# Performance work log

Hardware: AMD Instinct MI355X
Metric: run time of the kernel (lower is better)

## Reference

```python
import jax, jax.numpy as jnp
import numpy as np

N, F_IN, H, C, E, K = 100000, 128, 512, 16, 3200000, 3
EPS = 1e-5


def setup_inputs() -> dict:
    key = jax.random.key(0)
    ks = jax.random.split(key, 12)
    x = jax.random.normal(ks[0], (N, F_IN), jnp.float32)
    edge_index = jax.random.randint(ks[1], (2, E), 0, N, jnp.int64)
    # TAGConv has K+1 hop linears (bias folded into one vector, like PyG)
    W1 = jax.random.normal(ks[2], (K + 1, F_IN, H), jnp.float32) * 0.02
    b1 = jnp.zeros((H,), jnp.float32)
    W2 = jax.random.normal(ks[3], (K + 1, H, H), jnp.float32) * 0.02
    b2 = jnp.zeros((H,), jnp.float32)
    W3 = jax.random.normal(ks[4], (K + 1, H, C), jnp.float32) * 0.02
    b3 = jnp.zeros((C,), jnp.float32)
    gn1_w = jnp.ones((H,), jnp.float32)
    gn1_b = jnp.zeros((H,), jnp.float32)
    gn1_a = jnp.ones((H,), jnp.float32)  # mean_scale alpha
    gn2_w = jnp.ones((H,), jnp.float32)
    gn2_b = jnp.zeros((H,), jnp.float32)
    gn2_a = jnp.ones((H,), jnp.float32)
    return {"x": x, "edge_index": edge_index,
            "W1": W1, "b1": b1, "W2": W2, "b2": b2, "W3": W3, "b3": b3,
            "gn1_w": gn1_w, "gn1_b": gn1_b, "gn1_a": gn1_a,
            "gn2_w": gn2_w, "gn2_b": gn2_b, "gn2_a": gn2_a}


def _gcn_norm(edge_index, n):
    # PyG TAGConv: gcn_norm with add_self_loops=False, all-ones edge weights
    row, col = edge_index[0], edge_index[1]  # source j, target i
    deg = jax.ops.segment_sum(jnp.ones((edge_index.shape[1],), jnp.float32), col,
                              num_segments=n)
    dinv = jnp.where(deg > 0, jax.lax.rsqrt(jnp.maximum(deg, 1.0)), 0.0)
    return row, col, dinv[row] * dinv[col]


def _prop(h, row, col, norm, n):
    # out[i] = sum_{(j->i)} norm_e * h[j]
    return jax.ops.segment_sum(norm[:, None] * h[row], col, num_segments=n)


def _tagconv(x, row, col, norm, W, b):
    n = x.shape[0]
    out = x @ W[0]
    h = x
    for k in range(1, W.shape[0]):
        h = _prop(h, row, col, norm, n)
        out = out + h @ W[k]
    return out + b


def _graphnorm(x, w, b, a):
    # single graph: per-graph mean/var over all nodes
    mean = jnp.mean(x, axis=0)
    sub = x - a * mean
    var = jnp.mean(sub * sub, axis=0)
    return sub * jax.lax.rsqrt(var + EPS) * w + b


def reference(x, edge_index, W1, b1, W2, b2, W3, b3,
              gn1_w, gn1_b, gn1_a, gn2_w, gn2_b, gn2_a):
    n = x.shape[0]
    row, col, norm = _gcn_norm(edge_index, n)
    h = jax.nn.relu(_tagconv(x, row, col, norm, W1, b1))
    h = _graphnorm(h, gn1_w, gn1_b, gn1_a)
    h = jax.nn.relu(_tagconv(h, row, col, norm, W2, b2))
    h = _graphnorm(h, gn2_w, gn2_b, gn2_a)
    return _tagconv(h, row, col, norm, W3, b3)
```

## Files before the change

kernel.cpp:

```cpp
#include <hip/hip_runtime.h>

#define NN 100000
#define EE 3200000
#define EPSF 1e-5f

typedef unsigned short u16;
typedef short bf16x8 __attribute__((ext_vector_type(8)));
typedef float f32x4 __attribute__((ext_vector_type(4)));

static inline int cdiv(int a, int b) { return (a + b - 1) / b; }

__device__ __forceinline__ float b2f(u16 u) {
    return __uint_as_float((unsigned int)u << 16);
}
__device__ __forceinline__ u16 f2b(float f) {
    unsigned int i = __float_as_uint(f);
    return (u16)((i + 0x7FFFu + ((i >> 16) & 1u)) >> 16);
}
__device__ __forceinline__ int ep_src(unsigned int p) { return (int)(p & 0x1FFFFu); }
__device__ __forceinline__ float ep_w(unsigned int p) {
    return __uint_as_float(p & 0xFFFE0000u);
}
__device__ __forceinline__ unsigned pkhi(float f0, float f1) {
    return __builtin_amdgcn_perm(__float_as_uint(f1), __float_as_uint(f0), 0x07060302u);
}

__global__ void k_init(int* __restrict__ deg, int* __restrict__ cursor,
                       float* __restrict__ stats) {
    int i = blockIdx.x * 256 + threadIdx.x;
    if (i < NN) {
        deg[i] = 0;
        cursor[i] = 0;
    }
    if (i < 2048) stats[i] = 0.f;
}

__global__ void k_deg(const int* __restrict__ col, int* __restrict__ deg) {
    int i = blockIdx.x * 256 + threadIdx.x;
    if (i < EE) atomicAdd(&deg[col[i]], 1);
}

__global__ void k_dinv(const int* __restrict__ deg, float* __restrict__ dinv) {
    int i = blockIdx.x * 256 + threadIdx.x;
    if (i < NN) {
        int d = deg[i];
        dinv[i] = d > 0 ? rsqrtf((float)d) : 0.f;
    }
}

__global__ void k_scan(const int* __restrict__ deg, int* __restrict__ offs) {
    __shared__ int sh[1024];
    int tid = threadIdx.x;
    int start = tid * 98;
    int end = min(start + 98, NN);
    int sum = 0;
    for (int i = start; i < end; ++i) sum += deg[i];
    sh[tid] = sum;
    __syncthreads();
    for (int off = 1; off < 1024; off <<= 1) {
        int t = (tid >= off) ? sh[tid - off] : 0;
        __syncthreads();
        sh[tid] += t;
        __syncthreads();
    }
    int base = tid ? sh[tid - 1] : 0;
    for (int i = start; i < end; ++i) {
        offs[i] = base;
        base += deg[i];
    }
    if (tid == 1023) offs[NN] = sh[1023];
}

__global__ void k_scatter(const int* __restrict__ row, const int* __restrict__ col,
                          const float* __restrict__ dinv, const int* __restrict__ offs,
                          int* __restrict__ cursor, unsigned int* __restrict__ ep) {
    int i = blockIdx.x * 256 + threadIdx.x;
    if (i < EE) {
        int c = col[i], r = row[i];
        int pos = offs[c] + atomicAdd(&cursor[c], 1);
        float w = dinv[r] * dinv[c];
        unsigned int u = __float_as_uint(w);
        unsigned int rb = (u + 0xFFFFu + ((u >> 17) & 1u)) & 0xFFFE0000u;
        ep[pos] = rb | (unsigned int)r;
    }
}

__global__ void k_cvt(const float* __restrict__ src, u16* __restrict__ dst, int n4) {
    int idx = blockIdx.x * 256 + threadIdx.x;
    if (idx >= n4) return;
    float4 v = ((const float4*)src)[idx];
    ushort4 o;
    o.x = f2b(v.x);
    o.y = f2b(v.y);
    o.z = f2b(v.z);
    o.w = f2b(v.w);
    ((ushort4*)dst)[idx] = o;
}

__global__ void k_cvt8s(const u16* __restrict__ src, int lds_, unsigned char* __restrict__ dst,
                        int ldd) {
    int idx = blockIdx.x * 256 + threadIdx.x;
    if (idx >= NN * 128) return;
    int node = idx >> 7, f2 = (idx & 127) << 1;
    ushort2 v = *(const ushort2*)(src + (size_t)node * lds_ + f2);
    int pk = __builtin_amdgcn_cvt_pk_fp8_f32(b2f(v.x), b2f(v.y), 0, false);
    uchar2 o;
    o.x = (unsigned char)(pk & 0xFF);
    o.y = (unsigned char)((pk >> 8) & 0xFF);
    *(uchar2*)(dst + (size_t)node * ldd + f2) = o;
}

template <int S8>
__global__ void k_prop_t(const void* __restrict__ in, int ldin,
                         unsigned char* __restrict__ out8, int ldo8,
                         const int* __restrict__ offs, const unsigned int* __restrict__ ep) {
    int node = blockIdx.x;
    int f2 = threadIdx.x << 1;
    int s = offs[node], e = offs[node + 1];
    const u16* inb = (const u16*)in;
    const unsigned char* in8 = (const unsigned char*)in;
    float a0 = 0.f, a1 = 0.f;
    int t = s;
    for (; t + 4 <= e; t += 4) {
        unsigned int p0 = ep[t], p1 = ep[t + 1], p2 = ep[t + 2], p3 = ep[t + 3];
        float x0, y0, x1, y1, x2, y2, x3, y3;
        if (S8) {
            uchar2 c0 = *(const uchar2*)(in8 + (size_t)ep_src(p0) * ldin + f2);
            uchar2 c1 = *(const uchar2*)(in8 + (size_t)ep_src(p1) * ldin + f2);
            uchar2 c2 = *(const uchar2*)(in8 + (size_t)ep_src(p2) * ldin + f2);
            uchar2 c3 = *(const uchar2*)(in8 + (size_t)ep_src(p3) * ldin + f2);
            int w0 = c0.x | (c0.y << 8), w1 = c1.x | (c1.y << 8);
            int w2 = c2.x | (c2.y << 8), w3 = c3.x | (c3.y << 8);
            x0 = __builtin_amdgcn_cvt_f32_fp8(w0, 0);
            y0 = __builtin_amdgcn_cvt_f32_fp8(w0, 1);
            x1 = __builtin_amdgcn_cvt_f32_fp8(w1, 0);
            y1 = __builtin_amdgcn_cvt_f32_fp8(w1, 1);
            x2 = __builtin_amdgcn_cvt_f32_fp8(w2, 0);
            y2 = __builtin_amdgcn_cvt_f32_fp8(w2, 1);
            x3 = __builtin_amdgcn_cvt_f32_fp8(w3, 0);
            y3 = __builtin_amdgcn_cvt_f32_fp8(w3, 1);
        } else {
            ushort2 v0 = *(const ushort2*)(inb + (size_t)ep_src(p0) * ldin + f2);
            ushort2 v1 = *(const ushort2*)(inb + (size_t)ep_src(p1) * ldin + f2);
            ushort2 v2 = *(const ushort2*)(inb + (size_t)ep_src(p2) * ldin + f2);
            ushort2 v3 = *(const ushort2*)(inb + (size_t)ep_src(p3) * ldin + f2);
            x0 = b2f(v0.x);
            y0 = b2f(v0.y);
            x1 = b2f(v1.x);
            y1 = b2f(v1.y);
            x2 = b2f(v2.x);
            y2 = b2f(v2.y);
            x3 = b2f(v3.x);
            y3 = b2f(v3.y);
        }
        float w0 = ep_w(p0), w1 = ep_w(p1), w2 = ep_w(p2), w3 = ep_w(p3);
        a0 = fmaf(w0, x0, a0);
        a1 = fmaf(w0, y0, a1);
        a0 = fmaf(w1, x1, a0);
        a1 = fmaf(w1, y1, a1);
        a0 = fmaf(w2, x2, a0);
        a1 = fmaf(w2, y2, a1);
        a0 = fmaf(w3, x3, a0);
        a1 = fmaf(w3, y3, a1);
    }
    for (; t < e; ++t) {
        unsigned int p0 = ep[t];
        float x0, y0;
        if (S8) {
            uchar2 c0 = *(const uchar2*)(in8 + (size_t)ep_src(p0) * ldin + f2);
            int w = c0.x | (c0.y << 8);
            x0 = __builtin_amdgcn_cvt_f32_fp8(w, 0);
            y0 = __builtin_amdgcn_cvt_f32_fp8(w, 1);
        } else {
            ushort2 v0 = *(const ushort2*)(inb + (size_t)ep_src(p0) * ldin + f2);
            x0 = b2f(v0.x);
            y0 = b2f(v0.y);
        }
        float w0 = ep_w(p0);
        a0 = fmaf(w0, x0, a0);
        a1 = fmaf(w0, y0, a1);
    }
    int pk = __builtin_amdgcn_cvt_pk_fp8_f32(a0, a1, 0, false);
    uchar2 o8;
    o8.x = (unsigned char)(pk & 0xFF);
    o8.y = (unsigned char)((pk >> 8) & 0xFF);
    *(uchar2*)(out8 + (size_t)node * ldo8 + f2) = o8;
}

__global__ void k_prop256(const unsigned char* __restrict__ in, int ldin,
                          unsigned char* __restrict__ out, int ldout,
                          const int* __restrict__ offs, const unsigned int* __restrict__ ep) {
    int node = blockIdx.x;
    int f4 = threadIdx.x << 2;
    int s = offs[node], e = offs[node + 1];
    float a0 = 0, a1 = 0, a2 = 0, a3 = 0;
    int t = s;
    for (; t + 4 <= e; t += 4) {
        unsigned int p[4];
        unsigned int v[4];
#pragma unroll
        for (int u = 0; u < 4; ++u) p[u] = ep[t + u];
#pragma unroll
        for (int u = 0; u < 4; ++u)
            v[u] = *(const unsigned int*)(in + (size_t)ep_src(p[u]) * ldin + f4);
#pragma unroll
        for (int u = 0; u < 4; ++u) {
            float w = ep_w(p[u]);
            a0 = fmaf(w, __builtin_amdgcn_cvt_f32_fp8((int)v[u], 0), a0);
            a1 = fmaf(w, __builtin_amdgcn_cvt_f32_fp8((int)v[u], 1), a1);
            a2 = fmaf(w, __builtin_amdgcn_cvt_f32_fp8((int)v[u], 2), a2);
            a3 = fmaf(w, __builtin_amdgcn_cvt_f32_fp8((int)v[u], 3), a3);
        }
    }
    for (; t < e; ++t) {
        unsigned int p0 = ep[t];
        unsigned int v = *(const unsigned int*)(in + (size_t)ep_src(p0) * ldin + f4);
        float w = ep_w(p0);
        a0 = fmaf(w, __builtin_amdgcn_cvt_f32_fp8((int)v, 0), a0);
        a1 = fmaf(w, __builtin_amdgcn_cvt_f32_fp8((int)v, 1), a1);
        a2 = fmaf(w, __builtin_amdgcn_cvt_f32_fp8((int)v, 2), a2);
        a3 = fmaf(w, __builtin_amdgcn_cvt_f32_fp8((int)v, 3), a3);
    }
    int p01 = __builtin_amdgcn_cvt_pk_fp8_f32(a0, a1, 0, false);
    int p23 = __builtin_amdgcn_cvt_pk_fp8_f32(a2, a3, 0, false);
    unsigned int o = (unsigned)(p01 & 0xFFFF) | ((unsigned)p23 << 16);
    *(unsigned int*)(out + (size_t)node * ldout + f4) = o;
}

__global__ void k_prop16(const float* __restrict__ in, int ldin,
                         const float* __restrict__ add, int ldadd,
                         float* __restrict__ out, const float* __restrict__ bias,
                         const int* __restrict__ offs, const unsigned int* __restrict__ ep) {
    int node = blockIdx.x * 16 + (threadIdx.x >> 4);
    if (node >= NN) return;
    int f = threadIdx.x & 15;
    float acc = add[(size_t)node * ldadd + f];
    int s = offs[node], e = offs[node + 1];
    int t = s;
    for (; t + 8 <= e; t += 8) {
        unsigned int p[8];
        float v[8];
#pragma unroll
        for (int u = 0; u < 8; ++u) p[u] = ep[t + u];
#pragma unroll
        for (int u = 0; u < 8; ++u) v[u] = in[(size_t)ep_src(p[u]) * ldin + f];
#pragma unroll
        for (int u = 0; u < 8; ++u) acc = fmaf(ep_w(p[u]), v[u], acc);
    }
    for (; t < e; ++t) {
        unsigned int p0 = ep[t];
        acc = fmaf(ep_w(p0), in[(size_t)ep_src(p0) * ldin + f], acc);
    }
    if (bias) acc += bias[f];
    out[node * 16 + f] = acc;
}

#define LDS_LD 40
#define SWZ(r, ko) ((ko) ^ ((((r) >> 3) & 1) << 3))
__global__ __launch_bounds__(256) void k_gemm_mfma(
    const void* __restrict__ A0, int lda0, const void* __restrict__ A1, int lda1,
    const void* __restrict__ A2, int lda2, const void* __restrict__ A3, int lda3, int a8mask,
    const u16* __restrict__ B0, const u16* __restrict__ B1, const u16* __restrict__ B2,
    const u16* __restrict__ B3, int ldb, void* __restrict__ Cv, int ldc, int M, int Ktot,
    int Kq, const float* __restrict__ bias, int relu, int cmode,
    float* __restrict__ statsOut) {
    __shared__ u16 As[128 * LDS_LD];
    __shared__ u16 Bs[64 * LDS_LD];
    __shared__ float sstat[128];
    int tid = threadIdx.x;
    int wave = tid >> 6, lane = tid & 63;
    int quad = lane >> 4, lq = lane & 15;
    int m0 = blockIdx.y * 128, n0 = blockIdx.x * 64;
    f32x4 acc[2][4] = {};
    if (statsOut && tid < 128) sstat[tid] = 0.f;

    for (int ks = 0; ks < Ktot; ks += 32) {
        int src = ks / Kq;
        int kk = ks - src * Kq;
        const void* Ap = src == 0 ? A0 : src == 1 ? A1 : src == 2 ? A2 : A3;
        int lda = src == 0 ? lda0 : src == 1 ? lda1 : src == 2 ? lda2 : lda3;
        const u16* Bp = src == 0 ? B0 : src == 1 ? B1 : src == 2 ? B2 : B3;
        if ((a8mask >> src) & 1) {
            const unsigned char* A8 = (const unsigned char*)Ap;
#pragma unroll
            for (int i = 0; i < 2; ++i) {
                int s = tid + i * 256;
                int r = s >> 2, ko = (s & 3) << 3;
                int gr = m0 + r;
                if (gr > M - 1) gr = M - 1;
                uint2 w = *(const uint2*)(A8 + (size_t)gr * lda + kk + ko);
                float f0 = __builtin_amdgcn_cvt_f32_fp8((int)w.x, 0);
                float f1 = __builtin_amdgcn_cvt_f32_fp8((int)w.x, 1);
                float f2_ = __builtin_amdgcn_cvt_f32_fp8((int)w.x, 2);
                float f3 = __builtin_amdgcn_cvt_f32_fp8((int)w.x, 3);
                float f4 = __builtin_amdgcn_cvt_f32_fp8((int)w.y, 0);
                float f5 = __builtin_amdgcn_cvt_f32_fp8((int)w.y, 1);
                float f6 = __builtin_amdgcn_cvt_f32_fp8((int)w.y, 2);
                float f7 = __builtin_amdgcn_cvt_f32_fp8((int)w.y, 3);
                uint4 o;
                o.x = pkhi(f0, f1);
                o.y = pkhi(f2_, f3);
                o.z = pkhi(f4, f5);
                o.w = pkhi(f6, f7);
                *(uint4*)&As[r * LDS_LD + SWZ(r, ko)] = o;
            }
        } else {
            const u16* Ab = (const u16*)Ap;
#pragma unroll
            for (int i = 0; i < 2; ++i) {
                int s = tid + i * 256;
                int r = s >> 2, ko = (s & 3) << 3;
                int gr = m0 + r;
                if (gr > M - 1) gr = M - 1;
                uint4 v = *(const uint4*)(Ab + (size_t)gr * lda + kk + ko);
                *(uint4*)&As[r * LDS_LD + SWZ(r, ko)] = v;
            }
        }
        {
            int n = tid >> 2, ko = (tid & 3) << 3;
            uint4 v = *(const uint4*)(Bp + (size_t)(n0 + n) * ldb + kk + ko);
            *(uint4*)&Bs[n * LDS_LD + SWZ(n, ko)] = v;
        }
        __syncthreads();
        bf16x8 af[2], bfr[4];
#pragma unroll
        for (int i = 0; i < 2; ++i) {
            int r = wave * 32 + i * 16 + lq;
            af[i] = *(bf16x8*)&As[r * LDS_LD + SWZ(r, quad * 8)];
        }
#pragma unroll
        for (int j = 0; j < 4; ++j) {
            int r = j * 16 + lq;
            bfr[j] = *(bf16x8*)&Bs[r * LDS_LD + SWZ(r, quad * 8)];
        }
#pragma unroll
        for (int i = 0; i < 2; ++i)
#pragma unroll
            for (int j = 0; j < 4; ++j)
                acc[i][j] = __builtin_amdgcn_mfma_f32_16x16x32_bf16(af[i], bfr[j], acc[i][j],
                                                                    0, 0, 0);
        __syncthreads();
    }
#pragma unroll
    for (int i = 0; i < 2; ++i) {
#pragma unroll
        for (int j = 0; j < 4; ++j) {
            int c = n0 + j * 16 + lq;
            float bcol = bias ? bias[c] : 0.f;
            int rbase = m0 + wave * 32 + i * 16 + quad * 4;
            float ls = 0.f, lq2 = 0.f;
#pragma unroll
            for (int reg = 0; reg < 4; ++reg) {
                int r = rbase + reg;
                if (r >= M) continue;
                float t = acc[i][j][reg];
                if (cmode == 2) t += b2f(*((u16*)Cv + (size_t)r * ldc + c));
                t += bcol;
                if (relu) t = fmaxf(t, 0.f);
                if (cmode == 0)
                    ((float*)Cv)[(size_t)r * ldc + c] = t;
                else
                    *((u16*)Cv + (size_t)r * ldc + c) = f2b(t);
                ls += t;
                lq2 += t * t;
            }
            if (statsOut) {
                int jc = j * 16 + lq;
                atomicAdd(&sstat[jc], ls);
                atomicAdd(&sstat[64 + jc], lq2);
            }
        }
    }
    if (statsOut) {
        __syncthreads();
        if (tid < 64) atomicAdd(&statsOut[n0 + tid], sstat[tid]);
        else if (tid < 128) atomicAdd(&statsOut[512 + n0 + (tid - 64)], sstat[tid]);
    }
}

__global__ void k_gnorm(u16* __restrict__ X, int ld, const float* __restrict__ stats,
                        const float* __restrict__ w, const float* __restrict__ b,
                        const float* __restrict__ a) {
    int i = blockIdx.x;
    int c = threadIdx.x * 2;
    const float invn = 1.f / NN;
    ushort2 v = *(ushort2*)(X + (size_t)i * ld + c);
    float x0 = b2f(v.x), x1 = b2f(v.y);
    {
        float m = stats[c] * invn, q = stats[512 + c] * invn, al = a[c];
        float var = q - (2.f * al - al * al) * m * m;
        x0 = (x0 - al * m) * rsqrtf(var + EPSF) * w[c] + b[c];
    }
    {
        int c1 = c + 1;
        float m = stats[c1] * invn, q = stats[512 + c1] * invn, al = a[c1];
        float var = q - (2.f * al - al * al) * m * m;
        x1 = (x1 - al * m) * rsqrtf(var + EPSF) * w[c1] + b[c1];
    }
    v.x = f2b(x0);
    v.y = f2b(x1);
    *(ushort2*)(X + (size_t)i * ld + c) = v;
}

__global__ void k_wt(const float* __restrict__ src, u16* __restrict__ dst, int I, int O,
                     int total) {
    int idx = blockIdx.x * 256 + threadIdx.x;
    if (idx >= total) return;
    int io = I * O;
    int k = idx / io, rem = idx - k * io;
    int n = rem / I, i = rem - n * I;
    dst[idx] = f2b(src[(size_t)k * io + (size_t)i * O + n]);
}

__global__ void k_wt3(const float* __restrict__ W3, u16* __restrict__ W3T) {
    int idx = blockIdx.x * 256 + threadIdx.x;
    if (idx >= 64 * 512) return;
    int n = idx >> 9, i = idx & 511;
    int k = n >> 4, f = n & 15;
    W3T[idx] = f2b(W3[((size_t)k * 512 + i) * 16 + f]);
}

extern "C" void kernel_launch(void* const* d_in, const int* in_sizes, int n_in,
                              void* d_out, int out_size, void* d_ws, size_t ws_size,
                              hipStream_t stream) {
    const float* x = (const float*)d_in[0];
    const int* ei = (const int*)d_in[1];
    const float* W1 = (const float*)d_in[2];
    const float* b1 = (const float*)d_in[3];
    const float* W2 = (const float*)d_in[4];
    const float* b2 = (const float*)d_in[5];
    const float* W3 = (const float*)d_in[6];
    const float* b3 = (const float*)d_in[7];
    const float* g1w = (const float*)d_in[8];
    const float* g1b = (const float*)d_in[9];
    const float* g1a = (const float*)d_in[10];
    const float* g2w = (const float*)d_in[11];
    const float* g2b = (const float*)d_in[12];
    const float* g2a = (const float*)d_in[13];
    const int* row = ei;
    const int* col = ei + EE;

    char* p = (char*)d_ws;
    auto alloc = [&](size_t bytes) {
        char* r = p;
        p += (bytes + 255) & ~(size_t)255;
        return r;
    };
    u16* H1 = (u16*)alloc((size_t)NN * 512 * 2);
    u16* Y = (u16*)alloc((size_t)NN * 512 * 2);
    unsigned char* X8 = (unsigned char*)alloc((size_t)NN * 256);
    unsigned int* ep = (unsigned int*)alloc((size_t)EE * 4);
    u16* W1T = (u16*)alloc((size_t)4 * 512 * 128 * 2);
    u16* W2T = (u16*)alloc((size_t)4 * 512 * 512 * 2);
    u16* W3T = (u16*)alloc(64 * 512 * 2);
    float* dinv = (float*)alloc((size_t)NN * 4);
    float* stats = (float*)alloc(2048 * 4);
    int* deg = (int*)alloc((size_t)NN * 4);
    int* offs = (int*)alloc((size_t)(NN + 1) * 4);
    int* cursor = (int*)alloc((size_t)NN * 4);
    (void)ws_size;
    (void)in_sizes;
    (void)n_in;
    (void)out_size;

    u16* xb = Y;
    unsigned char* F8a = (unsigned char*)Y + (size_t)NN * 256;
    unsigned char* F8b = (unsigned char*)Y + (size_t)NN * 256 + (size_t)NN * 128;

    k_init<<<cdiv(NN, 256), 256, 0, stream>>>(deg, cursor, stats);
    k_deg<<<cdiv(EE, 256), 256, 0, stream>>>(col, deg);
    k_dinv<<<cdiv(NN, 256), 256, 0, stream>>>(deg, dinv);
    k_scan<<<1, 1024, 0, stream>>>(deg, offs);
    k_scatter<<<cdiv(EE, 256), 256, 0, stream>>>(row, col, dinv, offs, cursor, ep);
    k_wt<<<cdiv(4 * 128 * 512, 256), 256, 0, stream>>>(W1, W1T, 128, 512, 4 * 128 * 512);
    k_wt<<<cdiv(4 * 512 * 512, 256), 256, 0, stream>>>(W2, W2T, 512, 512, 4 * 512 * 512);
    k_wt3<<<cdiv(64 * 512, 256), 256, 0, stream>>>(W3, W3T);

    dim3 gg(512 / 64, cdiv(NN, 128));
    const size_t WQ = (size_t)512 * 512;
    const size_t W1Q = (size_t)512 * 128;

    k_cvt<<<cdiv(NN * 32, 256), 256, 0, stream>>>(x, xb, NN * 32);
    k_prop_t<0><<<NN, 64, 0, stream>>>(xb, 128, F8a, 128, offs, ep);
    k_gemm_mfma<<<gg, 256, 0, stream>>>(xb, 128, F8a, 128, xb, 128, xb, 128, 2, W1T,
                                        W1T + W1Q, W1T, W1T, 128, H1, 512, NN, 256, 128,
                                        nullptr, 0, 1, nullptr);
    k_prop_t<1><<<NN, 64, 0, stream>>>(F8a, 128, F8b, 128, offs, ep);
    k_prop_t<1><<<NN, 64, 0, stream>>>(F8b, 128, F8a, 128, offs, ep);
    k_gemm_mfma<<<gg, 256, 0, stream>>>(F8b, 128, F8a, 128, xb, 128, xb, 128, 3,
                                        W1T + 2 * W1Q, W1T + 3 * W1Q, W1T, W1T, 128, H1, 512,
                                        NN, 256, 128, b1, 1, 2, stats);
    k_gnorm<<<NN, 256, 0, stream>>>(H1, 512, stats, g1w, g1b, g1a);

    for (int c = 0; c < 2; ++c) {
        u16* h1c = H1 + 256 * c;
        k_cvt8s<<<cdiv(NN * 128, 256), 256, 0, stream>>>(h1c, 512, X8, 256);
        k_gemm_mfma<<<gg, 256, 0, stream>>>(h1c, 512, h1c, 512, h1c, 512, h1c, 512, 0,
                                            W2T + 256 * c, W2T, W2T, W2T, 512, Y, 512, NN, 256,
                                            256, nullptr, 0, c == 0 ? 1 : 2, nullptr);
        unsigned char* hp1 = (unsigned char*)H1 + 512 * c;
        unsigned char* hp2 = hp1 + 256;
        k_prop256<<<NN, 64, 0, stream>>>(X8, 256, hp1, 1024, offs, ep);
        k_prop256<<<NN, 64, 0, stream>>>(hp1, 1024, hp2, 1024, offs, ep);
        k_prop256<<<NN, 64, 0, stream>>>(hp2, 1024, X8, 256, offs, ep);
        k_gemm_mfma<<<gg, 256, 0, stream>>>(hp1, 1024, hp2, 1024, X8, 256, X8, 256, 7,
                                            W2T + WQ + 256 * c, W2T + 2 * WQ + 256 * c,
                                            W2T + 3 * WQ + 256 * c, W2T, 512, Y, 512, NN, 768,
                                            256, (c == 1) ? b2 : nullptr, c == 1 ? 1 : 0, 2,
                                            (c == 1) ? (stats + 1024) : nullptr);
    }
    k_gnorm<<<NN, 256, 0, stream>>>(Y, 512, stats + 1024, g2w, g2b, g2a);

    float* G = (float*)H1;
    float* tA = (float*)X8;
    float* tB = tA + (size_t)NN * 16;
    {
        dim3 g3(1, cdiv(NN, 128));
        k_gemm_mfma<<<g3, 256, 0, stream>>>(Y, 512, Y, 512, Y, 512, Y, 512, 0, W3T, W3T, W3T,
                                            W3T, 512, G, 64, NN, 512, 512, nullptr, 0, 0,
                                            nullptr);
    }
    k_prop16<<<cdiv(NN, 16), 256, 0, stream>>>(G + 48, 64, G + 32, 64, tA, nullptr, offs, ep);
    k_prop16<<<cdiv(NN, 16), 256, 0, stream>>>(tA, 16, G + 16, 64, tB, nullptr, offs, ep);
    k_prop16<<<cdiv(NN, 16), 256, 0, stream>>>(tB, 16, G + 0, 64, (float*)d_out, b3, offs, ep);
}
```

Baseline: 2.792 ms.

## Enlarge GEMM tile to 128x128 and stage bf16 operands via direct global-to-LDS loads

The MFMA GEMM moves from a 128x64 block tile to 128x128 with a 2x2 wave layout, so each wave computes a 64x64 sub-tile and operands are reused more per LDS load. Bf16 A and B tiles are now loaded with global_load_lds straight into an unpadded, XOR-swizzled LDS layout instead of going through registers. The fp8 A path loads 16 bytes per thread. An Ncols bound is added so the narrow W3 GEMM stays correct. The aim is to cut global and LDS traffic per FLOP and the register-staging overhead. In exchange, the grid has half as many blocks and each thread holds more accumulator registers, which can lower occupancy.

```diff
diff --git a/kernel.cpp b/kernel.cpp
--- a/kernel.cpp
+++ b/kernel.cpp
@@ -255,104 +255,118 @@
     out[node * 16 + f] = acc;
 }
 
-#define LDS_LD 40
-#define SWZ(r, ko) ((ko) ^ ((((r) >> 3) & 1) << 3))
+__device__ __forceinline__ void stage_bf16(char* lds, const char* src, size_t rowB,
+                                           int colOff, int rowBase, int rowMax, int tid) {
+    int wave = tid >> 6, lane = tid & 63;
+#pragma unroll
+    for (int i = 0; i < 2; ++i) {
+        int L = i * 4096 + wave * 1024 + lane * 16;
+        int r = L >> 6;
+        int kog = (L & 63) ^ ((r & 3) << 4);
+        int gr = rowBase + r;
+        if (gr > rowMax) gr = rowMax;
+        const char* g = src + (size_t)gr * rowB + colOff + kog;
+        __builtin_amdgcn_global_load_lds(
+            (const __attribute__((address_space(1))) void*)g,
+            (__attribute__((address_space(3))) void*)(lds + i * 4096 + wave * 1024), 16, 0, 0);
+    }
+}
+
 __global__ __launch_bounds__(256) void k_gemm_mfma(
     const void* __restrict__ A0, int lda0, const void* __restrict__ A1, int lda1,
     const void* __restrict__ A2, int lda2, const void* __restrict__ A3, int lda3, int a8mask,
     const u16* __restrict__ B0, const u16* __restrict__ B1, const u16* __restrict__ B2,
-    const u16* __restrict__ B3, int ldb, void* __restrict__ Cv, int ldc, int M, int Ktot,
-    int Kq, const float* __restrict__ bias, int relu, int cmode,
+    const u16* __restrict__ B3, int ldb, void* __restrict__ Cv, int ldc, int M, int Ncols,
+    int Ktot, int Kq, const float* __restrict__ bias, int relu, int cmode,
     float* __restrict__ statsOut) {
-    __shared__ u16 As[128 * LDS_LD];
-    __shared__ u16 Bs[64 * LDS_LD];
-    __shared__ float sstat[128];
+    __shared__ __align__(16) u16 As[128 * 32];
+    __shared__ __align__(16) u16 Bs[128 * 32];
+    __shared__ float sstat[256];
+    char* AsB = (char*)As;
+    char* BsB = (char*)Bs;
     int tid = threadIdx.x;
     int wave = tid >> 6, lane = tid & 63;
     int quad = lane >> 4, lq = lane & 15;
-    int m0 = blockIdx.y * 128, n0 = blockIdx.x * 64;
-    f32x4 acc[2][4] = {};
-    if (statsOut && tid < 128) sstat[tid] = 0.f;
-
+    int wr = wave >> 1, wc = wave & 1;
+    int m0 = blockIdx.y * 128, n0 = blockIdx.x * 128;
+    f32x4 acc[4][4] = {};
+    if (statsOut) sstat[tid] = 0.f;
+
+    int src = 0, kk = 0;
     for (int ks = 0; ks < Ktot; ks += 32) {
-        int src = ks / Kq;
-        int kk = ks - src * Kq;
         const void* Ap = src == 0 ? A0 : src == 1 ? A1 : src == 2 ? A2 : A3;
         int lda = src == 0 ? lda0 : src == 1 ? lda1 : src == 2 ? lda2 : lda3;
         const u16* Bp = src == 0 ? B0 : src == 1 ? B1 : src == 2 ? B2 : B3;
         if ((a8mask >> src) & 1) {
             const unsigned char* A8 = (const unsigned char*)Ap;
-#pragma unroll
-            for (int i = 0; i < 2; ++i) {
-                int s = tid + i * 256;
-                int r = s >> 2, ko = (s & 3) << 3;
-                int gr = m0 + r;
-                if (gr > M - 1) gr = M - 1;
-                uint2 w = *(const uint2*)(A8 + (size_t)gr * lda + kk + ko);
-                float f0 = __builtin_amdgcn_cvt_f32_fp8((int)w.x, 0);
-                float f1 = __builtin_amdgcn_cvt_f32_fp8((int)w.x, 1);
-                float f2_ = __builtin_amdgcn_cvt_f32_fp8((int)w.x, 2);
-                float f3 = __builtin_amdgcn_cvt_f32_fp8((int)w.x, 3);
-                float f4 = __builtin_amdgcn_cvt_f32_fp8((int)w.y, 0);
-                float f5 = __builtin_amdgcn_cvt_f32_fp8((int)w.y, 1);
-                float f6 = __builtin_amdgcn_cvt_f32_fp8((int)w.y, 2);
-                float f7 = __builtin_amdgcn_cvt_f32_fp8((int)w.y, 3);
-                uint4 o;
-                o.x = pkhi(f0, f1);
-                o.y = pkhi(f2_, f3);
-                o.z = pkhi(f4, f5);
-                o.w = pkhi(f6, f7);
-                *(uint4*)&As[r * LDS_LD + SWZ(r, ko)] = o;
-            }
+            int r = tid >> 1, h = tid & 1;
+            int gr = m0 + r;
+            if (gr > M - 1) gr = M - 1;
+            uint4 wv = *(const uint4*)(A8 + (size_t)gr * lda + kk + h * 16);
+            uint4 lo, hi;
+            lo.x = pkhi(__builtin_amdgcn_cvt_f32_fp8((int)wv.x, 0),
+                        __builtin_amdgcn_cvt_f32_fp8((int)wv.x, 1));
+            lo.y = pkhi(__builtin_amdgcn_cvt_f32_fp8((int)wv.x, 2),
+                        __builtin_amdgcn_cvt_f32_fp8((int)wv.x, 3));
+            lo.z = pkhi(__builtin_amdgcn_cvt_f32_fp8((int)wv.y, 0),
+                        __builtin_amdgcn_cvt_f32_fp8((int)wv.y, 1));
+            lo.w = pkhi(__builtin_amdgcn_cvt_f32_fp8((int)wv.y, 2),
+                        __builtin_amdgcn_cvt_f32_fp8((int)wv.y, 3));
+            hi.x = pkhi(__builtin_amdgcn_cvt_f32_fp8((int)wv.z, 0),
+                        __builtin_amdgcn_cvt_f32_fp8((int)wv.z, 1));
+            hi.y = pkhi(__builtin_amdgcn_cvt_f32_fp8((int)wv.z, 2),
+                        __builtin_amdgcn_cvt_f32_fp8((int)wv.z, 3));
+            hi.z = pkhi(__builtin_amdgcn_cvt_f32_fp8((int)wv.w, 0),
+                        __builtin_amdgcn_cvt_f32_fp8((int)wv.w, 1));
+            hi.w = pkhi(__builtin_amdgcn_cvt_f32_fp8((int)wv.w, 2),
+                        __builtin_amdgcn_cvt_f32_fp8((int)wv.w, 3));
+            int s = (r & 3) << 4;
+            *(uint4*)(AsB + r * 64 + ((h * 32) ^ s)) = lo;
+            *(uint4*)(AsB + r * 64 + ((h * 32 + 16) ^ s)) = hi;
         } else {
-            const u16* Ab = (const u16*)Ap;
-#pragma unroll
-            for (int i = 0; i < 2; ++i) {
-                int s = tid + i * 256;
-                int r = s >> 2, ko = (s & 3) << 3;
-                int gr = m0 + r;
-                if (gr > M - 1) gr = M - 1;
-                uint4 v = *(const uint4*)(Ab + (size_t)gr * lda + kk + ko);
-                *(uint4*)&As[r * LDS_LD + SWZ(r, ko)] = v;
-            }
-        }
-        {
-            int n = tid >> 2, ko = (tid & 3) << 3;
-            uint4 v = *(const uint4*)(Bp + (size_t)(n0 + n) * ldb + kk + ko);
-            *(uint4*)&Bs[n * LDS_LD + SWZ(n, ko)] = v;
-        }
+            stage_bf16(AsB, (const char*)Ap, (size_t)lda * 2, kk * 2, m0, M - 1, tid);
+        }
+        stage_bf16(BsB, (const char*)Bp, (size_t)ldb * 2, kk * 2, n0, Ncols - 1, tid);
         __syncthreads();
-        bf16x8 af[2], bfr[4];
-#pragma unroll
-        for (int i = 0; i < 2; ++i) {
-            int r = wave * 32 + i * 16 + lq;
-            af[i] = *(bf16x8*)&As[r * LDS_LD + SWZ(r, quad * 8)];
+        bf16x8 af[4], bfr[4];
+#pragma unroll
+        for (int i = 0; i < 4; ++i) {
+            int r = wr * 64 + i * 16 + lq;
+            af[i] = *(bf16x8*)(AsB + r * 64 + ((quad * 16) ^ ((r & 3) << 4)));
         }
 #pragma unroll
         for (int j = 0; j < 4; ++j) {
-            int r = j * 16 + lq;
-            bfr[j] = *(bf16x8*)&Bs[r * LDS_LD + SWZ(r, quad * 8)];
-        }
-#pragma unroll
-        for (int i = 0; i < 2; ++i)
+            int n = wc * 64 + j * 16 + lq;
+            bfr[j] = *(bf16x8*)(BsB + n * 64 + ((quad * 16) ^ ((n & 3) << 4)));
+        }
+#pragma unroll
+        for (int i = 0; i < 4; ++i)
 #pragma unroll
             for (int j = 0; j < 4; ++j)
                 acc[i][j] = __builtin_amdgcn_mfma_f32_16x16x32_bf16(af[i], bfr[j], acc[i][j],
                                                                     0, 0, 0);
         __syncthreads();
-    }
-#pragma unroll
-    for (int i = 0; i < 2; ++i) {
+        kk += 32;
+        if (kk == Kq) {
+            kk = 0;
+            ++src;
+        }
+    }
+
+#pragma unroll
+    for (int i = 0; i < 4; ++i) {
 #pragma unroll
         for (int j = 0; j < 4; ++j) {
-            int c = n0 + j * 16 + lq;
-            float bcol = bias ? bias[c] : 0.f;
-            int rbase = m0 + wave * 32 + i * 16 + quad * 4;
+            int jc = wc * 64 + j * 16 + lq;
+            int c = n0 + jc;
+            bool cok = c < Ncols;
+            float bcol = (bias && cok) ? bias[c] : 0.f;
+            int rbase = m0 + wr * 64 + i * 16 + quad * 4;
             float ls = 0.f, lq2 = 0.f;
 #pragma unroll
             for (int reg = 0; reg < 4; ++reg) {
                 int r = rbase + reg;
-                if (r >= M) continue;
+                if (r >= M || !cok) continue;
                 float t = acc[i][j][reg];
                 if (cmode == 2) t += b2f(*((u16*)Cv + (size_t)r * ldc + c));
                 t += bcol;
@@ -364,17 +378,18 @@
                 ls += t;
                 lq2 += t * t;
             }
-            if (statsOut) {
-                int jc = j * 16 + lq;
+            if (statsOut && cok) {
                 atomicAdd(&sstat[jc], ls);
-                atomicAdd(&sstat[64 + jc], lq2);
+                atomicAdd(&sstat[128 + jc], lq2);
             }
         }
     }
     if (statsOut) {
         __syncthreads();
-        if (tid < 64) atomicAdd(&statsOut[n0 + tid], sstat[tid]);
-        else if (tid < 128) atomicAdd(&statsOut[512 + n0 + (tid - 64)], sstat[tid]);
+        if (tid < 128)
+            atomicAdd(&statsOut[n0 + tid], sstat[tid]);
+        else
+            atomicAdd(&statsOut[512 + n0 + (tid - 128)], sstat[tid]);
     }
 }
 
@@ -476,28 +491,28 @@
     k_wt<<<cdiv(4 * 512 * 512, 256), 256, 0, stream>>>(W2, W2T, 512, 512, 4 * 512 * 512);
     k_wt3<<<cdiv(64 * 512, 256), 256, 0, stream>>>(W3, W3T);
 
-    dim3 gg(512 / 64, cdiv(NN, 128));
+    dim3 gg(512 / 128, cdiv(NN, 128));
     const size_t WQ = (size_t)512 * 512;
     const size_t W1Q = (size_t)512 * 128;
 
     k_cvt<<<cdiv(NN * 32, 256), 256, 0, stream>>>(x, xb, NN * 32);
     k_prop_t<0><<<NN, 64, 0, stream>>>(xb, 128, F8a, 128, offs, ep);
     k_gemm_mfma<<<gg, 256, 0, stream>>>(xb, 128, F8a, 128, xb, 128, xb, 128, 2, W1T,
-                                        W1T + W1Q, W1T, W1T, 128, H1, 512, NN, 256, 128,
+                                        W1T + W1Q, W1T, W1T, 128, H1, 512, NN, 512, 256, 128,
                                         nullptr, 0, 1, nullptr);
     k_prop_t<1><<<NN, 64, 0, stream>>>(F8a, 128, F8b, 128, offs, ep);
     k_prop_t<1><<<NN, 64, 0, stream>>>(F8b, 128, F8a, 128, offs, ep);
     k_gemm_mfma<<<gg, 256, 0, stream>>>(F8b, 128, F8a, 128, xb, 128, xb, 128, 3,
                                         W1T + 2 * W1Q, W1T + 3 * W1Q, W1T, W1T, 128, H1, 512,
-                                        NN, 256, 128, b1, 1, 2, stats);
+                                        NN, 512, 256, 128, b1, 1, 2, stats);
     k_gnorm<<<NN, 256, 0, stream>>>(H1, 512, stats, g1w, g1b, g1a);
 
     for (int c = 0; c < 2; ++c) {
         u16* h1c = H1 + 256 * c;
         k_cvt8s<<<cdiv(NN * 128, 256), 256, 0, stream>>>(h1c, 512, X8, 256);
         k_gemm_mfma<<<gg, 256, 0, stream>>>(h1c, 512, h1c, 512, h1c, 512, h1c, 512, 0,
-                                            W2T + 256 * c, W2T, W2T, W2T, 512, Y, 512, NN, 256,
-                                            256, nullptr, 0, c == 0 ? 1 : 2, nullptr);
+                                            W2T + 256 * c, W2T, W2T, W2T, 512, Y, 512, NN, 512,
+                                            256, 256, nullptr, 0, c == 0 ? 1 : 2, nullptr);
         unsigned char* hp1 = (unsigned char*)H1 + 512 * c;
         unsigned char* hp2 = hp1 + 256;
         k_prop256<<<NN, 64, 0, stream>>>(X8, 256, hp1, 1024, offs, ep);
@@ -505,9 +520,9 @@
         k_prop256<<<NN, 64, 0, stream>>>(hp2, 1024, X8, 256, offs, ep);
         k_gemm_mfma<<<gg, 256, 0, stream>>>(hp1, 1024, hp2, 1024, X8, 256, X8, 256, 7,
                                             W2T + WQ + 256 * c, W2T + 2 * WQ + 256 * c,
-                                            W2T + 3 * WQ + 256 * c, W2T, 512, Y, 512, NN, 768,
-                                            256, (c == 1) ? b2 : nullptr, c == 1 ? 1 : 0, 2,
-                                            (c == 1) ? (stats + 1024) : nullptr);
+                                            W2T + 3 * WQ + 256 * c, W2T, 512, Y, 512, NN, 512,
+                                            768, 256, (c == 1) ? b2 : nullptr, c == 1 ? 1 : 0,
+                                            2, (c == 1) ? (stats + 1024) : nullptr);
     }
     k_gnorm<<<NN, 256, 0, stream>>>(Y, 512, stats + 1024, g2w, g2b, g2a);
 
@@ -517,7 +532,7 @@
     {
         dim3 g3(1, cdiv(NN, 128));
         k_gemm_mfma<<<g3, 256, 0, stream>>>(Y, 512, Y, 512, Y, 512, Y, 512, 0, W3T, W3T, W3T,
-                                            W3T, 512, G, 64, NN, 512, 512, nullptr, 0, 0,
+                                            W3T, 512, G, 64, NN, 64, 512, 512, nullptr, 0, 0,
                                             nullptr);
     }
     k_prop16<<<cdiv(NN, 16), 256, 0, stream>>>(G + 48, 64, G + 32, 64, tA, nullptr, offs, ep);
```

Result: no change. 2.776 ms (-0.6%).
